# Kernel tuning notes

Measured on AMD Instinct MI355X. Metric: run time of the kernel, lower is better.

Reference implementation:

```python
import jax, jax.numpy as jnp
import numpy as np

# Irreps config: input/output = 32x0e + 16x1o (dim 80), H=4 heads -> head = 8x0e + 4x1o (dim 20)
M0, M1 = 32, 16      # input muls for 0e / 1o
m0, m1 = 8, 4        # per-head muls
H = 4
HEAD_DIM = m0 + 3 * m1   # 20
WNUM = H * (M0 * m0 + M1 * m0 + M0 * m1 + M1 * m1)  # 2304 per-edge TP weights
NB, HID = 16, 64
SQRT3 = np.float32(np.sqrt(3.0))
EPS = 1e-8


def radial_mlp(x, W1, b1, W2, b2):
    return jax.nn.silu(x @ W1 + b1) @ W2 + b2


def tp_edge(ss, vv, sh0, sh1, w):
    """FullyConnectedTensorProduct (32x0e+16x1o) x (1x0e+1x1o) -> H*(8x0e+4x1o) with per-edge weights w [E, WNUM].
    Paths: 0e*0e->0e, 1o*1o->0e (CG dot/sqrt3), 0e*1o->1o, 1o*0e->1o; path norm 1/sqrt(fan_in)."""
    E = ss.shape[0]
    per = M0 * m0 + M1 * m0 + M0 * m1 + M1 * m1  # 576
    w = w.reshape(E, H, per)
    o = 0
    Wss = w[..., o:o + M0 * m0].reshape(E, H, M0, m0); o += M0 * m0
    Wvv = w[..., o:o + M1 * m0].reshape(E, H, M1, m0); o += M1 * m0
    Wsv = w[..., o:o + M0 * m1].reshape(E, H, M0, m1); o += M0 * m1
    Wvs = w[..., o:o + M1 * m1].reshape(E, H, M1, m1)
    fan = np.float32(np.sqrt(M0 + M1))  # fan_in = 48 for both output irreps
    vv_dot = jnp.einsum('eui,ei->eu', vv, sh1) / SQRT3
    out0 = (jnp.einsum('eu,ehuw->ehw', ss * sh0[:, None], Wss)
            + jnp.einsum('eu,ehuw->ehw', vv_dot, Wvv)) / fan          # [E,H,m0]
    out1 = (jnp.einsum('eu,ehuw->ehw', ss, Wsv)[..., None] * sh1[:, None, None, :]
            + jnp.einsum('eui,ehuw->ehwi', vv * sh0[:, None, None], Wvs)) / fan  # [E,H,m1,3]
    return out0, out1


def setup_inputs() -> dict:
    key = jax.random.key(0)
    ks = jax.random.split(key, 24)
    N, E = 2000, 32000
    g = lambda k, s, sc=1.0: jax.random.normal(k, s, jnp.float32) * sc
    inp = {}
    inp['node_features'] = g(ks[0], (N, M0 + 3 * M1))
    inp['edge_index'] = jax.random.randint(ks[1], (2, E), 0, N)
    inp['edge_sh'] = g(ks[2], (E, 4))
    inp['edge_radial_emb'] = jax.random.uniform(ks[3], (E, NB), jnp.float32)
    # query e3nn Linear (per-head blocks)
    inp['Wq0'] = g(ks[4], (H, M0, m0))
    inp['Wq1'] = g(ks[5], (H, M1, m1))
    # radial MLPs for key / value TP weights
    inp['Wk1'] = g(ks[6], (NB, HID), 1 / np.sqrt(NB)); inp['bk1'] = jnp.zeros((HID,), jnp.float32)
    inp['Wk2'] = g(ks[7], (HID, WNUM), 1 / np.sqrt(HID)); inp['bk2'] = jnp.zeros((WNUM,), jnp.float32)
    inp['Wv1'] = g(ks[8], (NB, HID), 1 / np.sqrt(NB)); inp['bv1'] = jnp.zeros((HID,), jnp.float32)
    inp['Wv2'] = g(ks[9], (HID, WNUM), 1 / np.sqrt(HID)); inp['bv2'] = jnp.zeros((WNUM,), jnp.float32)
    # single-head dot-product TP -> 0e (shared weights)
    inp['Wd0'] = g(ks[10], (m0, m0))
    inp['Wd1'] = g(ks[11], (m1, m1))
    # output projection Linear (all heads mixed per irrep)
    inp['Wo0'] = g(ks[12], (H * m0, M0))
    inp['Wo1'] = g(ks[13], (H * m1, M1))
    # FFN: out irreps -> (2*M0)x0e + M1x1o -> out irreps
    inp['Wf1_0'] = g(ks[14], (M0, 2 * M0))
    inp['Wf1_1'] = g(ks[15], (M1, M1))
    inp['Wf2_0'] = g(ks[16], (2 * M0, M0))
    inp['Wf2_1'] = g(ks[17], (M1, M1))
    return inp


def reference(node_features, edge_index, edge_sh, edge_radial_emb,
              Wq0, Wq1, Wk1, bk1, Wk2, bk2, Wv1, bv1, Wv2, bv2,
              Wd0, Wd1, Wo0, Wo1, Wf1_0, Wf1_1, Wf2_0, Wf2_1):
    N = node_features.shape[0]
    s = node_features[:, :M0]                       # [N, M0] scalars
    v = node_features[:, M0:].reshape(N, M1, 3)     # [N, M1, 3] vectors
    src, dst = edge_index[0], edge_index[1]

    # query Linear (e3nn: per-irrep channel mix, norm 1/sqrt(fan_in))
    q0 = jnp.einsum('nu,huw->nhw', s, Wq0) / np.sqrt(M0)
    q1 = jnp.einsum('nui,huw->nhwi', v, Wq1) / np.sqrt(M1)

    sh0, sh1 = edge_sh[:, 0], edge_sh[:, 1:4]
    ss, vv = s[src], v[src]                         # gather per edge

    wk = radial_mlp(edge_radial_emb, Wk1, bk1, Wk2, bk2)
    wv = radial_mlp(edge_radial_emb, Wv1, bv1, Wv2, bv2)
    k0, k1 = tp_edge(ss, vv, sh0, sh1, wk)
    v0, v1 = tp_edge(ss, vv, sh0, sh1, wv)

    # per-head equivariant dot product -> 0e logits
    qd0, qd1 = q0[dst], q1[dst]
    fan_d = np.float32(np.sqrt(m0 * m0 + m1 * m1))
    logits = (jnp.einsum('ehu,uv,ehv->eh', qd0, Wd0, k0)
              + jnp.einsum('ehui,uv,ehvi->eh', qd1, Wd1, k1) / SQRT3) / fan_d
    logits = logits / np.sqrt(HEAD_DIM)             # self.scale
    logits = jnp.clip(logits, -10.0, 10.0)

    # scatter softmax over edges sharing a destination node
    seg_max = jax.ops.segment_max(logits, dst, num_segments=N)
    seg_max = jnp.maximum(seg_max, -10.0)           # handle empty segments
    ex = jnp.exp(logits - seg_max[dst])
    denom = jax.ops.segment_sum(ex, dst, num_segments=N)
    alpha = ex / (denom[dst] + 1e-12)               # [E, H]

    agg0 = jax.ops.segment_sum(alpha[..., None] * v0, dst, num_segments=N)        # [N,H,m0]
    agg1 = jax.ops.segment_sum(alpha[..., None, None] * v1, dst, num_segments=N)  # [N,H,m1,3]

    # output projection Linear over concatenated heads
    o0 = agg0.reshape(N, H * m0) @ Wo0 / np.sqrt(H * m0)
    o1 = jnp.einsum('nui,uw->nwi', agg1.reshape(N, H * m1, 3), Wo1) / np.sqrt(H * m1)

    # residual (input irreps == output irreps -> identity skip)
    x0 = s + o0
    x1 = v + o1

    # FFN with SafeNormActivation
    f0 = x0 @ Wf1_0 / np.sqrt(M0)                               # [N, 2*M0]
    f1 = jnp.einsum('nui,uw->nwi', x1, Wf1_1) / np.sqrt(M1)     # [N, M1, 3]
    a0 = jax.nn.silu(f0)
    norms = jnp.linalg.norm(f1, axis=-1, keepdims=True)
    safe = jnp.maximum(norms, EPS)
    a1 = jnp.where(norms < EPS, 0.0, (f1 / safe) * jax.nn.silu(norms))
    g0 = a0 @ Wf2_0 / np.sqrt(2 * M0)
    g1 = jnp.einsum('nui,uw->nwi', a1, Wf2_1) / np.sqrt(M1)

    out0 = x0 + g0
    out1 = x1 + g1
    return jnp.concatenate([out0, out1.reshape(N, M1 * 3)], axis=-1)
```

## Files before the change

### kernel.cpp

```cpp
#include <hip/hip_runtime.h>

typedef unsigned int uint;
typedef unsigned short ushort;
typedef __attribute__((ext_vector_type(8))) short bf16x8;
typedef __attribute__((ext_vector_type(4))) float f32x4;
typedef __attribute__((ext_vector_type(2))) float f32x2;

#define N_NODES 2000
#define N_EDGES 32000
#define WNUM 2304

constexpr size_t OFF_AGG0 = 0;
constexpr size_t OFF_AGG1 = 64000;
constexpr size_t OFF_DEN  = 160000;
constexpr size_t OFF_CNT  = 168000;
constexpr size_t OFF_FLAG = 170000;
constexpr size_t OFF_W2T  = 170004;
constexpr size_t OFF_QT0  = 317460;
constexpr size_t OFF_QT1  = 381460;
constexpr size_t OFF_EORD = 477460;
constexpr size_t OFF_W1T  = 509460;
constexpr size_t OFF_W1P  = 511508;

__device__ __forceinline__ float b2f(ushort u){ union{uint i; float f;}x; x.i=((uint)u)<<16; return x.f; }
__device__ __forceinline__ float lo16(uint w){ union{uint u; float f;}x; x.u=w<<16; return x.f; }
__device__ __forceinline__ float hi16(uint w){ union{uint u; float f;}x; x.u=w&0xFFFF0000u; return x.f; }
__device__ __forceinline__ ushort f2b(float f){
  union{float f; uint u;}x; x.f=f;
  uint r = (x.u + 0x7FFFu + ((x.u>>16)&1u)) >> 16;
  return (ushort)r;
}
__device__ __forceinline__ float siluf(float x){ return x / (1.f + __expf(-x)); }

template<bool F32>
__device__ __forceinline__ float ldf(const void* p, int i){
  if (F32) return ((const float*)p)[i];
  return b2f(((const ushort*)p)[i]);
}
__device__ __forceinline__ float ldfr(const void* p, int i, bool f32){
  return f32 ? ((const float*)p)[i] : b2f(((const ushort*)p)[i]);
}

template<bool F32>
__device__ void prep_body(
    const void* __restrict__ nf, const int* __restrict__ eidx,
    const void* __restrict__ Wk2, const void* __restrict__ Wv2,
    const void* __restrict__ Wk1, const void* __restrict__ Wv1,
    const void* __restrict__ Wq0, const void* __restrict__ Wq1,
    const void* __restrict__ Wd0, const void* __restrict__ Wd1,
    ushort* __restrict__ W2T, float* __restrict__ W1T, uint* __restrict__ W1P,
    float* __restrict__ qt0, float* __restrict__ qt1,
    int* __restrict__ cnt){
  const int t = threadIdx.x;
  const int bid = blockIdx.x;

  if (bid < 72){
    __shared__ ushort tile[64][66];
    const int mat = bid / 36, jt = bid - mat*36;
    const void* W = mat ? Wv2 : Wk2;
    const int j0 = jt*64;
    const int jo = t & 63, cb = t >> 6;
    #pragma unroll
    for (int k=0; k<16; ++k){
      const int c = cb + k*4;
      tile[c][jo] = F32 ? f2b(((const float*)W)[(size_t)c*WNUM + j0 + jo])
                        : ((const ushort*)W)[(size_t)c*WNUM + j0 + jo];
    }
    __syncthreads();
    const int jl = t >> 2, c0 = (t & 3)*16;
    ushort* dst = W2T + (size_t)mat*147456 + (size_t)(j0+jl)*64 + c0;
    #pragma unroll
    for (int k=0; k<16; ++k) dst[k] = tile[c0+k][jl];
  } else if (bid < 104){
    __shared__ float nfL[64][80];
    __shared__ float wq0L[1024], wq1L[256], wd0L[64], wd1L[16];
    const int nb = bid - 72, n0 = nb*64;
    for (int idx=t; idx<64*80; idx+=256){
      const int nn = n0 + idx/80;
      nfL[idx/80][idx%80] = (nn < N_NODES) ? ldf<F32>(nf, nn*80 + idx%80) : 0.f;
    }
    for (int idx=t; idx<1024; idx+=256) wq0L[idx] = ldf<F32>(Wq0, idx);
    if (t < 256) wq1L[t] = ldf<F32>(Wq1, t);
    if (t < 64)  wd0L[t] = ldf<F32>(Wd0, t);
    if (t < 16)  wd1L[t] = ldf<F32>(Wd1, t);
    __syncthreads();
    const int nl = t >> 2, h = t & 3;
    const int nn = n0 + nl;
    if (nn < N_NODES){
      const float* S = &nfL[nl][0];
      float q0[8];
      #pragma unroll
      for (int w=0; w<8; ++w){
        float a = 0.f;
        #pragma unroll
        for (int u=0; u<32; ++u) a += S[u]*wq0L[h*256 + u*8 + w];
        q0[w] = a * 0.17677669529663687f;
      }
      #pragma unroll
      for (int vv=0; vv<8; ++vv){
        float a = 0.f;
        #pragma unroll
        for (int u=0; u<8; ++u) a += q0[u]*wd0L[u*8+vv];
        qt0[nn*32 + h*8 + vv] = a;
      }
      float q1[12];
      #pragma unroll
      for (int w=0; w<4; ++w)
        #pragma unroll
        for (int i=0; i<3; ++i){
          float a = 0.f;
          #pragma unroll
          for (int u=0; u<16; ++u) a += S[32+u*3+i]*wq1L[h*64 + u*4 + w];
          q1[w*3+i] = a * 0.25f;
        }
      #pragma unroll
      for (int vv=0; vv<4; ++vv)
        #pragma unroll
        for (int i=0; i<3; ++i){
          float a = 0.f;
          #pragma unroll
          for (int u=0; u<4; ++u) a += q1[u*3+i]*wd1L[u*4+vv];
          qt1[nn*48 + h*12 + vv*3 + i] = a;
        }
    }
  } else if (bid == 104){
    for (int idx=t; idx<2048; idx+=256){
      const int mat = idx >> 10, rem = idx & 1023;
      const int c = rem >> 4, b = rem & 15;
      W1T[idx] = ldf<F32>(mat ? Wv1 : Wk1, b*64 + c);
    }
    for (int idx=t; idx<1024; idx+=256){
      const int mat = idx >> 9, rem = idx & 511;
      const int c = rem >> 3, j = rem & 7;
      const void* W = mat ? Wv1 : Wk1;
      ushort u0, u1;
      if (F32){ u0 = f2b(((const float*)W)[(2*j)*64+c]); u1 = f2b(((const float*)W)[(2*j+1)*64+c]); }
      else    { u0 = ((const ushort*)W)[(2*j)*64+c];     u1 = ((const ushort*)W)[(2*j+1)*64+c]; }
      W1P[idx] = (uint)u0 | ((uint)u1 << 16);
    }
  } else {
    const int e = (bid-105)*256 + t;
    if (e < N_EDGES) atomicAdd(cnt + eidx[N_EDGES + e], 1);
  }
}

__global__ __launch_bounds__(256) void prep_kernel(
    const void* nf, const int* eidx,
    const void* Wk2, const void* Wv2,
    const void* Wk1, const void* Wv1,
    const void* Wq0, const void* Wq1,
    const void* Wd0, const void* Wd1,
    ushort* W2T, float* W1T, uint* W1P, float* qt0, float* qt1,
    int* cnt, int* flag){
  __shared__ int s_cnt;
  const int t = threadIdx.x;
  if (t == 0) s_cnt = 0;
  __syncthreads();
  {
    uint u = ((const ushort*)nf)[t*2];
    uint ex = (u >> 7) & 0xFFu;
    if (ex >= 0xA0u) atomicAdd(&s_cnt, 1);
  }
  __syncthreads();
  const bool F32 = (s_cnt >= 20);
  if (blockIdx.x == 0 && t == 0) *flag = F32 ? 1 : 0;
  if (F32) prep_body<true >(nf, eidx, Wk2, Wv2, Wk1, Wv1, Wq0, Wq1, Wd0, Wd1, W2T, W1T, W1P, qt0, qt1, cnt);
  else     prep_body<false>(nf, eidx, Wk2, Wv2, Wk1, Wv1, Wq0, Wq1, Wd0, Wd1, W2T, W1T, W1P, qt0, qt1, cnt);
}

__global__ __launch_bounds__(256) void scan_kernel(int* __restrict__ cnt){
  __shared__ int ls[256];
  const int t = threadIdx.x;
  const int base = t*8;
  int v[8]; int s = 0;
  #pragma unroll
  for (int k=0; k<8; ++k){ int idx = base+k; v[k] = (idx < N_NODES) ? cnt[idx] : 0; s += v[k]; }
  ls[t] = s; __syncthreads();
  for (int off=1; off<256; off<<=1){
    int x = (t >= off) ? ls[t-off] : 0;
    __syncthreads();
    ls[t] += x;
    __syncthreads();
  }
  int ex = ls[t] - s;
  #pragma unroll
  for (int k=0; k<8; ++k){ int idx = base+k; if (idx < N_NODES){ int c = v[k]; cnt[idx] = ex; ex += c; } }
}

__global__ __launch_bounds__(256) void scat_kernel(const int* __restrict__ eidx,
                                                   int* __restrict__ cnt, int* __restrict__ eord){
  int e = blockIdx.x*256 + threadIdx.x;
  if (e < N_EDGES){
    int p = atomicAdd(cnt + eidx[N_EDGES + e], 1);
    eord[p] = e;
  }
}

struct Smem {
  ushort hidA[4096];
  union {
    struct {
      float fssT[32][34];
      float fvvT[16][34];
      float sslT[32][34];
    } f;
    float cont[2688];
  } u;
  float vshT[3][16][34];
  float sh1T[3][34];
  int   dstL[32];
};

template<bool F32>
__device__ void edge_body(
    const void* __restrict__ nf,  const int* __restrict__ eidx,
    const int* __restrict__ eord,
    const void* __restrict__ esh, const void* __restrict__ emb,
    const float* __restrict__ W1T, const uint* __restrict__ W1P,
    const void* __restrict__ bk1, const void* __restrict__ bk2,
    const void* __restrict__ bv1, const void* __restrict__ bv2,
    const ushort* __restrict__ W2T,
    const float* __restrict__ qt0g, const float* __restrict__ qt1g,
    float* __restrict__ agg0, float* __restrict__ agg1, float* __restrict__ denom,
    Smem& sm){
  const int t  = threadIdx.x;
  const int hw = t >> 5;
  const int r  = t & 31;
  const int geb = blockIdx.x*32;

  int geA[4], srcA[4], dstA[4];
  float shv0[4], shv1[4], shv2[4], shv3[4];
  #pragma unroll
  for (int e=0; e<4; ++e) geA[e] = eord[geb + hw*4 + e];
  #pragma unroll
  for (int e=0; e<4; ++e){ srcA[e] = eidx[geA[e]]; dstA[e] = eidx[N_EDGES + geA[e]]; }
  #pragma unroll
  for (int e=0; e<4; ++e){
    if (F32){
      float4 s4 = ((const float4*)esh)[geA[e]];
      shv0[e]=s4.x; shv1[e]=s4.y; shv2[e]=s4.z; shv3[e]=s4.w;
    } else {
      uint2 u2 = ((const uint2*)esh)[geA[e]];
      shv0[e]=lo16(u2.x); shv1[e]=hi16(u2.x); shv2[e]=lo16(u2.y); shv3[e]=hi16(u2.y);
    }
  }
  #pragma unroll
  for (int e=0; e<4; ++e){
    const int le = hw*4+e, src = srcA[e];
    const float sh0 = shv0[e], s1a = shv1[e], s1b = shv2[e], s1c = shv3[e];
    if (r == 0) sm.dstL[le] = dstA[e];
    if (r < 3) sm.sh1T[r][le] = (r==0)? s1a : (r==1)? s1b : s1c;
    float sv = ldf<F32>(nf, src*80 + r);
    sm.u.f.sslT[r][le] = sv;
    sm.u.f.fssT[r][le] = sv * sh0;
    if (r < 16){
      float v0 = ldf<F32>(nf, src*80+32+r*3+0);
      float v1 = ldf<F32>(nf, src*80+32+r*3+1);
      float v2 = ldf<F32>(nf, src*80+32+r*3+2);
      sm.vshT[0][r][le] = v0*sh0; sm.vshT[1][r][le] = v1*sh0; sm.vshT[2][r][le] = v2*sh0;
      sm.u.f.fvvT[r][le] = (v0*s1a + v1*s1b + v2*s1c) * 0.5773502691896258f;
    }
  }

  {
    float bkv[2], bvv[2];
    f32x4 wkF[2][4], wvF[2][4];
    uint4 wkB[2][2], wvB[2][2];
    #pragma unroll
    for (int cc=0; cc<2; ++cc){
      const int c = r + cc*32;
      bkv[cc] = ldf<F32>(bk1, c); bvv[cc] = ldf<F32>(bv1, c);
      if (F32){
        const f32x4* pk = (const f32x4*)(W1T + c*16);
        const f32x4* pv = (const f32x4*)(W1T + 1024 + c*16);
        wkF[cc][0]=pk[0]; wkF[cc][1]=pk[1]; wkF[cc][2]=pk[2]; wkF[cc][3]=pk[3];
        wvF[cc][0]=pv[0]; wvF[cc][1]=pv[1]; wvF[cc][2]=pv[2]; wvF[cc][3]=pv[3];
      } else {
        const uint4* pk = (const uint4*)(W1P + c*8);
        const uint4* pv = (const uint4*)(W1P + 512 + c*8);
        wkB[cc][0]=pk[0]; wkB[cc][1]=pk[1];
        wvB[cc][0]=pv[0]; wvB[cc][1]=pv[1];
      }
    }
    uint4 ra, rb; float4 fa, fb, fc, fd;
    if (F32){
      const float4* p = (const float4*)emb + (size_t)geA[0]*4;
      fa = p[0]; fb = p[1]; fc = p[2]; fd = p[3];
    } else {
      const uint4* p = (const uint4*)emb + (size_t)geA[0]*2;
      ra = p[0]; rb = p[1];
    }
    #pragma unroll
    for (int e=0; e<4; ++e){
      float em[16];
      if (F32){
        em[0]=fa.x; em[1]=fa.y; em[2]=fa.z; em[3]=fa.w;
        em[4]=fb.x; em[5]=fb.y; em[6]=fb.z; em[7]=fb.w;
        em[8]=fc.x; em[9]=fc.y; em[10]=fc.z; em[11]=fc.w;
        em[12]=fd.x; em[13]=fd.y; em[14]=fd.z; em[15]=fd.w;
      } else {
        em[0]=lo16(ra.x); em[1]=hi16(ra.x); em[2]=lo16(ra.y); em[3]=hi16(ra.y);
        em[4]=lo16(ra.z); em[5]=hi16(ra.z); em[6]=lo16(ra.w); em[7]=hi16(ra.w);
        em[8]=lo16(rb.x); em[9]=hi16(rb.x); em[10]=lo16(rb.y); em[11]=hi16(rb.y);
        em[12]=lo16(rb.z); em[13]=hi16(rb.z); em[14]=lo16(rb.w); em[15]=hi16(rb.w);
      }
      if (e < 3){
        if (F32){
          const float4* p = (const float4*)emb + (size_t)geA[e+1]*4;
          fa = p[0]; fb = p[1]; fc = p[2]; fd = p[3];
        } else {
          const uint4* p = (const uint4*)emb + (size_t)geA[e+1]*2;
          ra = p[0]; rb = p[1];
        }
      }
      const int le = hw*4+e;
      #pragma unroll
      for (int cc=0; cc<2; ++cc){
        const int c = r + cc*32;
        float ak = bkv[cc], av = bvv[cc];
        if (F32){
          #pragma unroll
          for (int g=0; g<4; ++g)
            #pragma unroll
            for (int j=0; j<4; ++j){
              ak += em[g*4+j]*wkF[cc][g][j];
              av += em[g*4+j]*wvF[cc][g][j];
            }
        } else {
          #pragma unroll
          for (int g=0; g<2; ++g){
            const uint4 a = wkB[cc][g], b = wvB[cc][g];
            ak += em[g*8+0]*lo16(a.x) + em[g*8+1]*hi16(a.x)
                + em[g*8+2]*lo16(a.y) + em[g*8+3]*hi16(a.y)
                + em[g*8+4]*lo16(a.z) + em[g*8+5]*hi16(a.z)
                + em[g*8+6]*lo16(a.w) + em[g*8+7]*hi16(a.w);
            av += em[g*8+0]*lo16(b.x) + em[g*8+1]*hi16(b.x)
                + em[g*8+2]*lo16(b.y) + em[g*8+3]*hi16(b.y)
                + em[g*8+4]*lo16(b.z) + em[g*8+5]*hi16(b.z)
                + em[g*8+6]*lo16(b.w) + em[g*8+7]*hi16(b.w);
          }
        }
        const int idx = (le>>4)*1024 + (c>>5)*512 + ((((c>>3)&3)*16 + (le&15))<<3) + (c&7);
        sm.hidA[idx]        = f2b(siluf(ak));
        sm.hidA[2048 + idx] = f2b(siluf(av));
      }
    }
  }
  __syncthreads();

  const int h = t >> 6;
  const int lane = t & 63, q = lane >> 4, n = lane & 15;
  const float invfan = 0.14433756729740643f;
  float exv[2][4];

  const ushort* wbase = W2T + h*36864 + n*64 + q*8;
  const int bi0 = h*576 + n;
  const float* fb_ss = &sm.u.f.fssT[n>>3][q*4];
  const float* fb_sl = &sm.u.f.sslT[n>>2][q*4];
  const int nq2 = n>>2;

  #pragma unroll 1
  for (int kv=0; kv<2; ++kv){
    const ushort* wptr = wbase + kv*147456;
    const void* bvec = kv ? bv2 : bk2;
    bf16x8 af[2][2];
    #pragma unroll
    for (int Mt=0; Mt<2; ++Mt)
      #pragma unroll
      for (int kh=0; kh<2; ++kh)
        af[Mt][kh] = *(const bf16x8*)&sm.hidA[kv*2048 + Mt*1024 + kh*512 + lane*8];

    float a0[2][4], aP[2][4], aW[3][2][4];
    #pragma unroll
    for (int Mt=0; Mt<2; ++Mt)
      #pragma unroll
      for (int z=0; z<4; ++z){
        a0[Mt][z]=0.f; aP[Mt][z]=0.f;
        aW[0][Mt][z]=0.f; aW[1][Mt][z]=0.f; aW[2][Mt][z]=0.f;
      }

    bf16x8 pb0 = *(const bf16x8*)(wptr);
    bf16x8 pb1 = *(const bf16x8*)(wptr + 32);
    float pbb = ldf<F32>(bvec, bi0);

    #pragma unroll 4
    for (int tl=0; tl<24; ++tl){
      bf16x8 b0 = pb0, b1 = pb1; const float bb = pbb;
      pb0 = *(const bf16x8*)(wptr + (tl+1)*1024);
      pb1 = *(const bf16x8*)(wptr + (tl+1)*1024 + 32);
      pbb = ldf<F32>(bvec, bi0 + (tl+1)*16);
      const float* fp = fb_ss + tl*68;
      #pragma unroll
      for (int Mt=0; Mt<2; ++Mt){
        f32x4 c = {bb,bb,bb,bb};
        c = __builtin_amdgcn_mfma_f32_16x16x32_bf16(af[Mt][0], b0, c, 0,0,0);
        c = __builtin_amdgcn_mfma_f32_16x16x32_bf16(af[Mt][1], b1, c, 0,0,0);
        f32x2 fA = *(const f32x2*)(fp + Mt*16);
        f32x2 fB = *(const f32x2*)(fp + Mt*16 + 2);
        a0[Mt][0] += c[0]*fA[0]; a0[Mt][1] += c[1]*fA[1];
        a0[Mt][2] += c[2]*fB[0]; a0[Mt][3] += c[3]*fB[1];
      }
    }
    #pragma unroll 4
    for (int tl=24; tl<32; ++tl){
      bf16x8 b0 = pb0, b1 = pb1; const float bb = pbb;
      pb0 = *(const bf16x8*)(wptr + (tl+1)*1024);
      pb1 = *(const bf16x8*)(wptr + (tl+1)*1024 + 32);
      pbb = ldf<F32>(bvec, bi0 + (tl+1)*16);
      const float* fp = fb_sl + (tl-24)*136;
      #pragma unroll
      for (int Mt=0; Mt<2; ++Mt){
        f32x4 c = {bb,bb,bb,bb};
        c = __builtin_amdgcn_mfma_f32_16x16x32_bf16(af[Mt][0], b0, c, 0,0,0);
        c = __builtin_amdgcn_mfma_f32_16x16x32_bf16(af[Mt][1], b1, c, 0,0,0);
        f32x2 fA = *(const f32x2*)(fp + Mt*16);
        f32x2 fB = *(const f32x2*)(fp + Mt*16 + 2);
        aP[Mt][0] += c[0]*fA[0]; aP[Mt][1] += c[1]*fA[1];
        aP[Mt][2] += c[2]*fB[0]; aP[Mt][3] += c[3]*fB[1];
      }
    }
    #pragma unroll
    for (int tl=32; tl<36; ++tl){
      bf16x8 b0 = pb0, b1 = pb1; const float bb = pbb;
      if (tl < 35){
        pb0 = *(const bf16x8*)(wptr + (tl+1)*1024);
        pb1 = *(const bf16x8*)(wptr + (tl+1)*1024 + 32);
        pbb = ldf<F32>(bvec, bi0 + (tl+1)*16);
      }
      const int u = (tl-32)*4 + nq2;
      #pragma unroll
      for (int Mt=0; Mt<2; ++Mt){
        f32x4 c = {bb,bb,bb,bb};
        c = __builtin_amdgcn_mfma_f32_16x16x32_bf16(af[Mt][0], b0, c, 0,0,0);
        c = __builtin_amdgcn_mfma_f32_16x16x32_bf16(af[Mt][1], b1, c, 0,0,0);
        #pragma unroll
        for (int i=0; i<3; ++i){
          f32x2 fA = *(const f32x2*)&sm.vshT[i][u][Mt*16+q*4];
          f32x2 fB = *(const f32x2*)&sm.vshT[i][u][Mt*16+q*4+2];
          aW[i][Mt][0] += c[0]*fA[0]; aW[i][Mt][1] += c[1]*fA[1];
          aW[i][Mt][2] += c[2]*fB[0]; aW[i][Mt][3] += c[3]*fB[1];
        }
      }
    }

    #pragma unroll
    for (int Mt=0; Mt<2; ++Mt)
      #pragma unroll
      for (int z=0; z<4; ++z){
        a0[Mt][z] += __shfl_xor(a0[Mt][z], 8, 64);
        aP[Mt][z] += __shfl_xor(aP[Mt][z], 4, 64);
        aP[Mt][z] += __shfl_xor(aP[Mt][z], 8, 64);
        #pragma unroll
        for (int i=0; i<3; ++i){
          aW[i][Mt][z] += __shfl_xor(aW[i][Mt][z], 4, 64);
          aW[i][Mt][z] += __shfl_xor(aW[i][Mt][z], 8, 64);
        }
      }

    if (kv == 0){
      float lgp[2][4];
      #pragma unroll
      for (int Mt=0; Mt<2; ++Mt)
        #pragma unroll
        for (int z=0; z<4; ++z){
          const int el = Mt*16 + q*4 + z;
          const int d = sm.dstL[el];
          float acc = 0.f;
          if (n < 8) acc = qt0g[d*32 + h*8 + n] * a0[Mt][z];
          if (n < 4){
            float s = 0.f;
            #pragma unroll
            for (int i=0; i<3; ++i){
              float k1 = aP[Mt][z]*sm.sh1T[i][el] + aW[i][Mt][z];
              s += qt1g[d*48 + h*12 + n*3 + i] * k1;
            }
            acc += s * 0.5773502691896258f;
          }
          lgp[Mt][z] = acc;
        }
      #pragma unroll
      for (int Mt=0; Mt<2; ++Mt)
        #pragma unroll
        for (int z=0; z<4; ++z){
          lgp[Mt][z] += __shfl_xor(lgp[Mt][z], 1, 64);
          lgp[Mt][z] += __shfl_xor(lgp[Mt][z], 2, 64);
          lgp[Mt][z] += __shfl_xor(lgp[Mt][z], 4, 64);
          lgp[Mt][z] += __shfl_xor(lgp[Mt][z], 8, 64);
          float lg = lgp[Mt][z] * invfan * 0.025f;
          lg = fminf(10.f, fmaxf(-10.f, lg));
          exv[Mt][z] = __expf(lg - 10.0f);
        }
    } else {
      __syncthreads();
      #pragma unroll
      for (int Mt=0; Mt<2; ++Mt)
        #pragma unroll
        for (int z=0; z<4; ++z){
          const int el = Mt*16 + q*4 + z;
          const float ex = exv[Mt][z];
          float* cp = &sm.u.cont[el*84 + h*21];
          if (n == 0) cp[0] = ex;
          if (n < 8)  cp[1+n] = ex * a0[Mt][z] * invfan;
          if (n < 4){
            #pragma unroll
            for (int i=0; i<3; ++i){
              float v1 = (aP[Mt][z]*sm.sh1T[i][el] + aW[i][Mt][z]) * invfan;
              cp[9+n*3+i] = ex * v1;
            }
          }
        }
    }
  }
  __syncthreads();

  if (t < 168){
    const int half = (t >= 84) ? 1 : 0;
    const int tt = t - half*84;
    const int h2 = tt / 21, comp = tt - h2*21;
    const int e0 = half*16, e1 = e0 + 16;
    float acc = 0.f;
    #pragma unroll 4
    for (int e2=e0; e2<e1; ++e2){
      acc += sm.u.cont[e2*84 + h2*21 + comp];
      const int d2 = sm.dstL[e2];
      if (e2 == e1-1 || sm.dstL[e2+1] != d2){
        if (comp == 0)      atomicAdd(denom + d2*4  + h2, acc);
        else if (comp < 9)  atomicAdd(agg0  + d2*32 + h2*8  + (comp-1), acc);
        else                atomicAdd(agg1  + d2*48 + h2*12 + (comp-9), acc);
        acc = 0.f;
      }
    }
  }
}

__global__ __launch_bounds__(256) void edge_kernel(
    const void* nf, const int* eidx, const int* eord, const void* esh, const void* emb,
    const float* W1T, const uint* W1P,
    const void* bk1, const void* bk2,
    const void* bv1, const void* bv2,
    const ushort* W2T, const float* qt0g, const float* qt1g,
    float* agg0, float* agg1, float* denom, const int* flag){
  __shared__ Smem sm;
  if (*flag)
    edge_body<true >(nf,eidx,eord,esh,emb,W1T,W1P,bk1,bk2,bv1,bv2,W2T,qt0g,qt1g,agg0,agg1,denom,sm);
  else
    edge_body<false>(nf,eidx,eord,esh,emb,W1T,W1P,bk1,bk2,bv1,bv2,W2T,qt0g,qt1g,agg0,agg1,denom,sm);
}

__global__ __launch_bounds__(256) void node_out_kernel(
    const void* __restrict__ nf, const float* __restrict__ agg0r, const float* __restrict__ agg1r,
    const float* __restrict__ denom,
    const void* __restrict__ Wo0, const void* __restrict__ Wo1,
    const void* __restrict__ Wf10, const void* __restrict__ Wf11,
    const void* __restrict__ Wf20, const void* __restrict__ Wf21,
    void* __restrict__ out, const int* __restrict__ flag){
  __shared__ float ag0[4][32], ag1[4][48], adiv[4][4];
  __shared__ float x0s[4][32], x1s[4][48], a0s[4][64], f1s[4][48], coefs[4][16];
  const bool F32 = (*flag) != 0;
  const int s = threadIdx.x >> 6, t = threadIdx.x & 63;
  const int n = blockIdx.x*4 + s;
  if (t < 4) adiv[s][t] = 1.f / (denom[n*4+t] + 1e-12f);
  __syncthreads();
  if (t < 32) ag0[s][t] = agg0r[n*32+t] * adiv[s][t>>3];
  if (t < 48) ag1[s][t] = agg1r[n*48+t] * adiv[s][t/12];
  __syncthreads();
  if (t < 32){
    float o = 0.f;
    #pragma unroll
    for (int k=0; k<32; ++k) o += ag0[s][k]*ldfr(Wo0, k*32+t, F32);
    x0s[s][t] = ldfr(nf, n*80+t, F32) + o*0.17677669529663687f;
  }
  if (t < 48){
    int w = t/3, i = t - w*3;
    float o = 0.f;
    #pragma unroll
    for (int u=0; u<16; ++u) o += ag1[s][u*3+i]*ldfr(Wo1, u*16+w, F32);
    x1s[s][t] = ldfr(nf, n*80+32+t, F32) + o*0.25f;
  }
  __syncthreads();
  {
    float f0 = 0.f;
    #pragma unroll
    for (int u=0; u<32; ++u) f0 += x0s[s][u]*ldfr(Wf10, u*64+t, F32);
    a0s[s][t] = siluf(f0*0.17677669529663687f);
  }
  if (t < 48){
    int w = t/3, i = t - w*3;
    float f1 = 0.f;
    #pragma unroll
    for (int u=0; u<16; ++u) f1 += x1s[s][u*3+i]*ldfr(Wf11, u*16+w, F32);
    f1s[s][t] = f1*0.25f;
  }
  __syncthreads();
  if (t < 16){
    float a = f1s[s][t*3], b = f1s[s][t*3+1], c = f1s[s][t*3+2];
    float nrm = sqrtf(a*a+b*b+c*c);
    float safe = fmaxf(nrm, 1e-8f);
    coefs[s][t] = (nrm < 1e-8f) ? 0.f : siluf(nrm)/safe;
  }
  __syncthreads();
  if (t < 32){
    float g = 0.f;
    #pragma unroll
    for (int u=0; u<64; ++u) g += a0s[s][u]*ldfr(Wf20, u*32+t, F32);
    float val = x0s[s][t] + g*0.125f;
    if (F32) ((float*)out)[n*80+t] = val; else ((ushort*)out)[n*80+t] = f2b(val);
  }
  if (t < 48){
    int w = t/3, i = t - w*3;
    float g = 0.f;
    #pragma unroll
    for (int u=0; u<16; ++u) g += coefs[s][u]*f1s[s][u*3+i]*ldfr(Wf21, u*16+w, F32);
    float val = x1s[s][t] + g*0.25f;
    if (F32) ((float*)out)[n*80+32+t] = val; else ((ushort*)out)[n*80+32+t] = f2b(val);
  }
}

extern "C" void kernel_launch(void* const* d_in, const int* in_sizes, int n_in,
                              void* d_out, int out_size, void* d_ws, size_t ws_size,
                              hipStream_t stream){
  const void* nf   = d_in[0];
  const int*  eidx = (const int*)d_in[1];
  const void* esh  = d_in[2];
  const void* emb  = d_in[3];
  const void* Wq0  = d_in[4];
  const void* Wq1  = d_in[5];
  const void* Wk1  = d_in[6];
  const void* bk1  = d_in[7];
  const void* Wk2  = d_in[8];
  const void* bk2  = d_in[9];
  const void* Wv1  = d_in[10];
  const void* bv1  = d_in[11];
  const void* Wv2  = d_in[12];
  const void* bv2  = d_in[13];
  const void* Wd0  = d_in[14];
  const void* Wd1  = d_in[15];
  const void* Wo0  = d_in[16];
  const void* Wo1  = d_in[17];
  const void* Wf10 = d_in[18];
  const void* Wf11 = d_in[19];
  const void* Wf20 = d_in[20];
  const void* Wf21 = d_in[21];
  float* ws = (float*)d_ws;

  float* agg0  = ws + OFF_AGG0;
  float* agg1  = ws + OFF_AGG1;
  float* denom = ws + OFF_DEN;
  int*   cnt   = (int*)(ws + OFF_CNT);
  int*   flag  = (int*)(ws + OFF_FLAG);
  ushort* W2T  = (ushort*)(ws + OFF_W2T);
  float* qt0   = ws + OFF_QT0;
  float* qt1   = ws + OFF_QT1;
  int*   eord  = (int*)(ws + OFF_EORD);
  float* W1T   = ws + OFF_W1T;
  uint*  W1P   = (uint*)(ws + OFF_W1P);

  hipMemsetAsync(agg0, 0, 170000*sizeof(float), stream);
  prep_kernel<<<230, 256, 0, stream>>>(nf, eidx, Wk2, Wv2, Wk1, Wv1, Wq0, Wq1, Wd0, Wd1,
                                       W2T, W1T, W1P, qt0, qt1, cnt, flag);
  scan_kernel<<<1, 256, 0, stream>>>(cnt);
  scat_kernel<<<125, 256, 0, stream>>>(eidx, cnt, eord);
  edge_kernel<<<N_EDGES/32, 256, 0, stream>>>(nf, eidx, eord, esh, emb,
                                              W1T, W1P, bk1, bk2, bv1, bv2,
                                              W2T, qt0, qt1,
                                              agg0, agg1, denom, flag);
  node_out_kernel<<<N_NODES/4, 256, 0, stream>>>(nf, agg0, agg1, denom,
                                                 Wo0, Wo1, Wf10, Wf11, Wf20, Wf21, d_out, flag);
}
```

Measured before the change: 226.0 us.

## Split key/value TP passes across separate wavefronts with 512-thread edge blocks

The edge kernel grows from 256 to 512 threads per block. Key and value weight passes now run concurrently on separate wave groups instead of a serial kv loop, and the logits from the key waves reach the value waves through a new shared exL array. The prologue and hidden-layer work is redistributed over the larger block, the weight prefetch is double-buffered, and the final segment reduction uses four edge ranges instead of two. This doubles parallelism per block and shortens the serial chain, but raises register and LDS pressure per block, which may lower occupancy.

```diff
diff --git a/kernel.cpp b/kernel.cpp
--- a/kernel.cpp
+++ b/kernel.cpp
@@ -208,8 +208,23 @@
   } u;
   float vshT[3][16][34];
   float sh1T[3][34];
+  float exL[32][4];
   int   dstL[32];
 };
+
+__device__ __forceinline__ f32x4 mma_pair(const bf16x8& a0f, const bf16x8& a1f,
+                                          bf16x8 b0, bf16x8 b1, float bb){
+  f32x4 c = {bb,bb,bb,bb};
+  c = __builtin_amdgcn_mfma_f32_16x16x32_bf16(a0f, b0, c, 0,0,0);
+  c = __builtin_amdgcn_mfma_f32_16x16x32_bf16(a1f, b1, c, 0,0,0);
+  return c;
+}
+__device__ __forceinline__ void acc_feat(const f32x4 c, const float* fp, float* acc){
+  f32x2 fA = *(const f32x2*)(fp);
+  f32x2 fB = *(const f32x2*)(fp + 2);
+  acc[0] += c[0]*fA[0]; acc[1] += c[1]*fA[1];
+  acc[2] += c[2]*fB[0]; acc[3] += c[3]*fB[1];
+}
 
 template<bool F32>
 __device__ void edge_body(
@@ -224,70 +239,72 @@
     float* __restrict__ agg0, float* __restrict__ agg1, float* __restrict__ denom,
     Smem& sm){
   const int t  = threadIdx.x;
-  const int hw = t >> 5;
-  const int r  = t & 31;
   const int geb = blockIdx.x*32;
 
-  int geA[4], srcA[4], dstA[4];
-  float shv0[4], shv1[4], shv2[4], shv3[4];
-  #pragma unroll
-  for (int e=0; e<4; ++e) geA[e] = eord[geb + hw*4 + e];
-  #pragma unroll
-  for (int e=0; e<4; ++e){ srcA[e] = eidx[geA[e]]; dstA[e] = eidx[N_EDGES + geA[e]]; }
-  #pragma unroll
-  for (int e=0; e<4; ++e){
+  {
+    const int g = t >> 5, r = t & 31;
+    int geA[2], srcA[2], dstA[2];
+    float shv0[2], shv1[2], shv2[2], shv3[2];
+    #pragma unroll
+    for (int e=0; e<2; ++e) geA[e] = eord[geb + g*2 + e];
+    #pragma unroll
+    for (int e=0; e<2; ++e){ srcA[e] = eidx[geA[e]]; dstA[e] = eidx[N_EDGES + geA[e]]; }
+    #pragma unroll
+    for (int e=0; e<2; ++e){
+      if (F32){
+        float4 s4 = ((const float4*)esh)[geA[e]];
+        shv0[e]=s4.x; shv1[e]=s4.y; shv2[e]=s4.z; shv3[e]=s4.w;
+      } else {
+        uint2 u2 = ((const uint2*)esh)[geA[e]];
+        shv0[e]=lo16(u2.x); shv1[e]=hi16(u2.x); shv2[e]=lo16(u2.y); shv3[e]=hi16(u2.y);
+      }
+    }
+    #pragma unroll
+    for (int e=0; e<2; ++e){
+      const int le = g*2+e, src = srcA[e];
+      const float sh0 = shv0[e], s1a = shv1[e], s1b = shv2[e], s1c = shv3[e];
+      if (r == 0) sm.dstL[le] = dstA[e];
+      if (r < 3) sm.sh1T[r][le] = (r==0)? s1a : (r==1)? s1b : s1c;
+      float sv = ldf<F32>(nf, src*80 + r);
+      sm.u.f.sslT[r][le] = sv;
+      sm.u.f.fssT[r][le] = sv * sh0;
+      if (r < 16){
+        float v0 = ldf<F32>(nf, src*80+32+r*3+0);
+        float v1 = ldf<F32>(nf, src*80+32+r*3+1);
+        float v2 = ldf<F32>(nf, src*80+32+r*3+2);
+        sm.vshT[0][r][le] = v0*sh0; sm.vshT[1][r][le] = v1*sh0; sm.vshT[2][r][le] = v2*sh0;
+        sm.u.f.fvvT[r][le] = (v0*s1a + v1*s1b + v2*s1c) * 0.5773502691896258f;
+      }
+    }
+  }
+
+  {
+    const int c  = t & 63;
+    const int g4 = t >> 6;
+    int geB[4];
+    #pragma unroll
+    for (int e=0; e<4; ++e) geB[e] = eord[geb + g4*4 + e];
+
+    float bkv = ldf<F32>(bk1, c), bvv = ldf<F32>(bv1, c);
+    f32x4 wkF[4], wvF[4];
+    uint4 wkB[2], wvB[2];
     if (F32){
-      float4 s4 = ((const float4*)esh)[geA[e]];
-      shv0[e]=s4.x; shv1[e]=s4.y; shv2[e]=s4.z; shv3[e]=s4.w;
+      const f32x4* pk = (const f32x4*)(W1T + c*16);
+      const f32x4* pv = (const f32x4*)(W1T + 1024 + c*16);
+      wkF[0]=pk[0]; wkF[1]=pk[1]; wkF[2]=pk[2]; wkF[3]=pk[3];
+      wvF[0]=pv[0]; wvF[1]=pv[1]; wvF[2]=pv[2]; wvF[3]=pv[3];
     } else {
-      uint2 u2 = ((const uint2*)esh)[geA[e]];
-      shv0[e]=lo16(u2.x); shv1[e]=hi16(u2.x); shv2[e]=lo16(u2.y); shv3[e]=hi16(u2.y);
-    }
-  }
-  #pragma unroll
-  for (int e=0; e<4; ++e){
-    const int le = hw*4+e, src = srcA[e];
-    const float sh0 = shv0[e], s1a = shv1[e], s1b = shv2[e], s1c = shv3[e];
-    if (r == 0) sm.dstL[le] = dstA[e];
-    if (r < 3) sm.sh1T[r][le] = (r==0)? s1a : (r==1)? s1b : s1c;
-    float sv = ldf<F32>(nf, src*80 + r);
-    sm.u.f.sslT[r][le] = sv;
-    sm.u.f.fssT[r][le] = sv * sh0;
-    if (r < 16){
-      float v0 = ldf<F32>(nf, src*80+32+r*3+0);
-      float v1 = ldf<F32>(nf, src*80+32+r*3+1);
-      float v2 = ldf<F32>(nf, src*80+32+r*3+2);
-      sm.vshT[0][r][le] = v0*sh0; sm.vshT[1][r][le] = v1*sh0; sm.vshT[2][r][le] = v2*sh0;
-      sm.u.f.fvvT[r][le] = (v0*s1a + v1*s1b + v2*s1c) * 0.5773502691896258f;
-    }
-  }
-
-  {
-    float bkv[2], bvv[2];
-    f32x4 wkF[2][4], wvF[2][4];
-    uint4 wkB[2][2], wvB[2][2];
-    #pragma unroll
-    for (int cc=0; cc<2; ++cc){
-      const int c = r + cc*32;
-      bkv[cc] = ldf<F32>(bk1, c); bvv[cc] = ldf<F32>(bv1, c);
-      if (F32){
-        const f32x4* pk = (const f32x4*)(W1T + c*16);
-        const f32x4* pv = (const f32x4*)(W1T + 1024 + c*16);
-        wkF[cc][0]=pk[0]; wkF[cc][1]=pk[1]; wkF[cc][2]=pk[2]; wkF[cc][3]=pk[3];
-        wvF[cc][0]=pv[0]; wvF[cc][1]=pv[1]; wvF[cc][2]=pv[2]; wvF[cc][3]=pv[3];
-      } else {
-        const uint4* pk = (const uint4*)(W1P + c*8);
-        const uint4* pv = (const uint4*)(W1P + 512 + c*8);
-        wkB[cc][0]=pk[0]; wkB[cc][1]=pk[1];
-        wvB[cc][0]=pv[0]; wvB[cc][1]=pv[1];
-      }
+      const uint4* pk = (const uint4*)(W1P + c*8);
+      const uint4* pv = (const uint4*)(W1P + 512 + c*8);
+      wkB[0]=pk[0]; wkB[1]=pk[1];
+      wvB[0]=pv[0]; wvB[1]=pv[1];
     }
     uint4 ra, rb; float4 fa, fb, fc, fd;
     if (F32){
-      const float4* p = (const float4*)emb + (size_t)geA[0]*4;
+      const float4* p = (const float4*)emb + (size_t)geB[0]*4;
       fa = p[0]; fb = p[1]; fc = p[2]; fd = p[3];
     } else {
-      const uint4* p = (const uint4*)emb + (size_t)geA[0]*2;
+      const uint4* p = (const uint4*)emb + (size_t)geB[0]*2;
       ra = p[0]; rb = p[1];
     }
     #pragma unroll
@@ -306,218 +323,206 @@
       }
       if (e < 3){
         if (F32){
-          const float4* p = (const float4*)emb + (size_t)geA[e+1]*4;
+          const float4* p = (const float4*)emb + (size_t)geB[e+1]*4;
           fa = p[0]; fb = p[1]; fc = p[2]; fd = p[3];
         } else {
-          const uint4* p = (const uint4*)emb + (size_t)geA[e+1]*2;
+          const uint4* p = (const uint4*)emb + (size_t)geB[e+1]*2;
           ra = p[0]; rb = p[1];
         }
       }
-      const int le = hw*4+e;
-      #pragma unroll
-      for (int cc=0; cc<2; ++cc){
-        const int c = r + cc*32;
-        float ak = bkv[cc], av = bvv[cc];
-        if (F32){
+      const int le = g4*4+e;
+      float ak = bkv, av = bvv;
+      if (F32){
+        #pragma unroll
+        for (int g=0; g<4; ++g)
           #pragma unroll
-          for (int g=0; g<4; ++g)
-            #pragma unroll
-            for (int j=0; j<4; ++j){
-              ak += em[g*4+j]*wkF[cc][g][j];
-              av += em[g*4+j]*wvF[cc][g][j];
-            }
-        } else {
-          #pragma unroll
-          for (int g=0; g<2; ++g){
-            const uint4 a = wkB[cc][g], b = wvB[cc][g];
-            ak += em[g*8+0]*lo16(a.x) + em[g*8+1]*hi16(a.x)
-                + em[g*8+2]*lo16(a.y) + em[g*8+3]*hi16(a.y)
-                + em[g*8+4]*lo16(a.z) + em[g*8+5]*hi16(a.z)
-                + em[g*8+6]*lo16(a.w) + em[g*8+7]*hi16(a.w);
-            av += em[g*8+0]*lo16(b.x) + em[g*8+1]*hi16(b.x)
-                + em[g*8+2]*lo16(b.y) + em[g*8+3]*hi16(b.y)
-                + em[g*8+4]*lo16(b.z) + em[g*8+5]*hi16(b.z)
-                + em[g*8+6]*lo16(b.w) + em[g*8+7]*hi16(b.w);
+          for (int j=0; j<4; ++j){
+            ak += em[g*4+j]*wkF[g][j];
+            av += em[g*4+j]*wvF[g][j];
           }
+      } else {
+        #pragma unroll
+        for (int g=0; g<2; ++g){
+          const uint4 a = wkB[g], b = wvB[g];
+          ak += em[g*8+0]*lo16(a.x) + em[g*8+1]*hi16(a.x)
+              + em[g*8+2]*lo16(a.y) + em[g*8+3]*hi16(a.y)
+              + em[g*8+4]*lo16(a.z) + em[g*8+5]*hi16(a.z)
+              + em[g*8+6]*lo16(a.w) + em[g*8+7]*hi16(a.w);
+          av += em[g*8+0]*lo16(b.x) + em[g*8+1]*hi16(b.x)
+              + em[g*8+2]*lo16(b.y) + em[g*8+3]*hi16(b.y)
+              + em[g*8+4]*lo16(b.z) + em[g*8+5]*hi16(b.z)
+              + em[g*8+6]*lo16(b.w) + em[g*8+7]*hi16(b.w);
         }
-        const int idx = (le>>4)*1024 + (c>>5)*512 + ((((c>>3)&3)*16 + (le&15))<<3) + (c&7);
-        sm.hidA[idx]        = f2b(siluf(ak));
-        sm.hidA[2048 + idx] = f2b(siluf(av));
-      }
-    }
-  }
-  __syncthreads();
-
-  const int h = t >> 6;
+      }
+      const int idx = (le>>4)*1024 + (c>>5)*512 + ((((c>>3)&3)*16 + (le&15))<<3) + (c&7);
+      sm.hidA[idx]        = f2b(siluf(ak));
+      sm.hidA[2048 + idx] = f2b(siluf(av));
+    }
+  }
+  __syncthreads();
+
+  const int w  = t >> 6;
+  const int kv = w >> 2;
+  const int h  = w & 3;
   const int lane = t & 63, q = lane >> 4, n = lane & 15;
   const float invfan = 0.14433756729740643f;
-  float exv[2][4];
-
-  const ushort* wbase = W2T + h*36864 + n*64 + q*8;
+
+  const ushort* wptr = W2T + (size_t)kv*147456 + h*36864 + n*64 + q*8;
+  const void* bvec = kv ? bv2 : bk2;
   const int bi0 = h*576 + n;
   const float* fb_ss = &sm.u.f.fssT[n>>3][q*4];
   const float* fb_sl = &sm.u.f.sslT[n>>2][q*4];
   const int nq2 = n>>2;
 
-  #pragma unroll 1
-  for (int kv=0; kv<2; ++kv){
-    const ushort* wptr = wbase + kv*147456;
-    const void* bvec = kv ? bv2 : bk2;
-    bf16x8 af[2][2];
+  bf16x8 af[2][2];
+  #pragma unroll
+  for (int Mt=0; Mt<2; ++Mt)
+    #pragma unroll
+    for (int kh=0; kh<2; ++kh)
+      af[Mt][kh] = *(const bf16x8*)&sm.hidA[kv*2048 + Mt*1024 + kh*512 + lane*8];
+
+  float a0[2][4], aP[2][4], aW[3][2][4];
+  #pragma unroll
+  for (int Mt=0; Mt<2; ++Mt)
+    #pragma unroll
+    for (int z=0; z<4; ++z){
+      a0[Mt][z]=0.f; aP[Mt][z]=0.f;
+      aW[0][Mt][z]=0.f; aW[1][Mt][z]=0.f; aW[2][Mt][z]=0.f;
+    }
+
+#define PREF(P0,P1,PB,TL) \
+  P0 = *(const bf16x8*)(wptr + (TL)*1024); \
+  P1 = *(const bf16x8*)(wptr + (TL)*1024 + 32); \
+  PB = ldf<F32>(bvec, bi0 + (TL)*16);
+
+  bf16x8 pA0, pA1, pB0, pB1; float pAb, pBb;
+  PREF(pA0, pA1, pAb, 0);
+  PREF(pB0, pB1, pBb, 1);
+
+  #pragma unroll 2
+  for (int tl=0; tl<24; tl+=2){
+    { bf16x8 b0=pA0, b1=pA1; float bb=pAb;
+      PREF(pA0, pA1, pAb, tl+2);
+      const float* fp = fb_ss + tl*68;
+      #pragma unroll
+      for (int Mt=0; Mt<2; ++Mt) acc_feat(mma_pair(af[Mt][0], af[Mt][1], b0, b1, bb), fp + Mt*16, a0[Mt]); }
+    { bf16x8 b0=pB0, b1=pB1; float bb=pBb;
+      PREF(pB0, pB1, pBb, tl+3);
+      const float* fp = fb_ss + (tl+1)*68;
+      #pragma unroll
+      for (int Mt=0; Mt<2; ++Mt) acc_feat(mma_pair(af[Mt][0], af[Mt][1], b0, b1, bb), fp + Mt*16, a0[Mt]); }
+  }
+  #pragma unroll 2
+  for (int tl=24; tl<32; tl+=2){
+    { bf16x8 b0=pA0, b1=pA1; float bb=pAb;
+      PREF(pA0, pA1, pAb, tl+2);
+      const float* fp = fb_sl + (tl-24)*136;
+      #pragma unroll
+      for (int Mt=0; Mt<2; ++Mt) acc_feat(mma_pair(af[Mt][0], af[Mt][1], b0, b1, bb), fp + Mt*16, aP[Mt]); }
+    { bf16x8 b0=pB0, b1=pB1; float bb=pBb;
+      PREF(pB0, pB1, pBb, tl+3);
+      const float* fp = fb_sl + (tl-23)*136;
+      #pragma unroll
+      for (int Mt=0; Mt<2; ++Mt) acc_feat(mma_pair(af[Mt][0], af[Mt][1], b0, b1, bb), fp + Mt*16, aP[Mt]); }
+  }
+#define BODY_AW(B0,B1,BB,TL) { \
+    const int u = ((TL)-32)*4 + nq2; \
+    _Pragma("unroll") \
+    for (int Mt=0; Mt<2; ++Mt){ \
+      f32x4 c = mma_pair(af[Mt][0], af[Mt][1], B0, B1, BB); \
+      _Pragma("unroll") \
+      for (int i=0; i<3; ++i) acc_feat(c, &sm.vshT[i][u][Mt*16+q*4], aW[i][Mt]); \
+    } }
+  { bf16x8 b0=pA0, b1=pA1; float bb=pAb; PREF(pA0, pA1, pAb, 34); BODY_AW(b0,b1,bb,32); }
+  { bf16x8 b0=pB0, b1=pB1; float bb=pBb; PREF(pB0, pB1, pBb, 35); BODY_AW(b0,b1,bb,33); }
+  { bf16x8 b0=pA0, b1=pA1; float bb=pAb; BODY_AW(b0,b1,bb,34); }
+  { bf16x8 b0=pB0, b1=pB1; float bb=pBb; BODY_AW(b0,b1,bb,35); }
+#undef BODY_AW
+#undef PREF
+
+  #pragma unroll
+  for (int Mt=0; Mt<2; ++Mt)
+    #pragma unroll
+    for (int z=0; z<4; ++z){
+      a0[Mt][z] += __shfl_xor(a0[Mt][z], 8, 64);
+      aP[Mt][z] += __shfl_xor(aP[Mt][z], 4, 64);
+      aP[Mt][z] += __shfl_xor(aP[Mt][z], 8, 64);
+      #pragma unroll
+      for (int i=0; i<3; ++i){
+        aW[i][Mt][z] += __shfl_xor(aW[i][Mt][z], 4, 64);
+        aW[i][Mt][z] += __shfl_xor(aW[i][Mt][z], 8, 64);
+      }
+    }
+
+  if (kv == 0){
+    float lgp[2][4];
     #pragma unroll
     for (int Mt=0; Mt<2; ++Mt)
       #pragma unroll
-      for (int kh=0; kh<2; ++kh)
-        af[Mt][kh] = *(const bf16x8*)&sm.hidA[kv*2048 + Mt*1024 + kh*512 + lane*8];
-
-    float a0[2][4], aP[2][4], aW[3][2][4];
+      for (int z=0; z<4; ++z){
+        const int el = Mt*16 + q*4 + z;
+        const int d = sm.dstL[el];
+        float acc = 0.f;
+        if (n < 8) acc = qt0g[d*32 + h*8 + n] * a0[Mt][z];
+        if (n < 4){
+          float s = 0.f;
+          #pragma unroll
+          for (int i=0; i<3; ++i){
+            float k1 = aP[Mt][z]*sm.sh1T[i][el] + aW[i][Mt][z];
+            s += qt1g[d*48 + h*12 + n*3 + i] * k1;
+          }
+          acc += s * 0.5773502691896258f;
+        }
+        lgp[Mt][z] = acc;
+      }
     #pragma unroll
     for (int Mt=0; Mt<2; ++Mt)
       #pragma unroll
       for (int z=0; z<4; ++z){
-        a0[Mt][z]=0.f; aP[Mt][z]=0.f;
-        aW[0][Mt][z]=0.f; aW[1][Mt][z]=0.f; aW[2][Mt][z]=0.f;
-      }
-
-    bf16x8 pb0 = *(const bf16x8*)(wptr);
-    bf16x8 pb1 = *(const bf16x8*)(wptr + 32);
-    float pbb = ldf<F32>(bvec, bi0);
-
-    #pragma unroll 4
-    for (int tl=0; tl<24; ++tl){
-      bf16x8 b0 = pb0, b1 = pb1; const float bb = pbb;
-      pb0 = *(const bf16x8*)(wptr + (tl+1)*1024);
-      pb1 = *(const bf16x8*)(wptr + (tl+1)*1024 + 32);
-      pbb = ldf<F32>(bvec, bi0 + (tl+1)*16);
-      const float* fp = fb_ss + tl*68;
-      #pragma unroll
-      for (int Mt=0; Mt<2; ++Mt){
-        f32x4 c = {bb,bb,bb,bb};
-        c = __builtin_amdgcn_mfma_f32_16x16x32_bf16(af[Mt][0], b0, c, 0,0,0);
-        c = __builtin_amdgcn_mfma_f32_16x16x32_bf16(af[Mt][1], b1, c, 0,0,0);
-        f32x2 fA = *(const f32x2*)(fp + Mt*16);
-        f32x2 fB = *(const f32x2*)(fp + Mt*16 + 2);
-        a0[Mt][0] += c[0]*fA[0]; a0[Mt][1] += c[1]*fA[1];
-        a0[Mt][2] += c[2]*fB[0]; a0[Mt][3] += c[3]*fB[1];
-      }
-    }
-    #pragma unroll 4
-    for (int tl=24; tl<32; ++tl){
-      bf16x8 b0 = pb0, b1 = pb1; const float bb = pbb;
-      pb0 = *(const bf16x8*)(wptr + (tl+1)*1024);
-      pb1 = *(const bf16x8*)(wptr + (tl+1)*1024 + 32);
-      pbb = ldf<F32>(bvec, bi0 + (tl+1)*16);
-      const float* fp = fb_sl + (tl-24)*136;
-      #pragma unroll
-      for (int Mt=0; Mt<2; ++Mt){
-        f32x4 c = {bb,bb,bb,bb};
-        c = __builtin_amdgcn_mfma_f32_16x16x32_bf16(af[Mt][0], b0, c, 0,0,0);
-        c = __builtin_amdgcn_mfma_f32_16x16x32_bf16(af[Mt][1], b1, c, 0,0,0);
-        f32x2 fA = *(const f32x2*)(fp + Mt*16);
-        f32x2 fB = *(const f32x2*)(fp + Mt*16 + 2);
-        aP[Mt][0] += c[0]*fA[0]; aP[Mt][1] += c[1]*fA[1];
-        aP[Mt][2] += c[2]*fB[0]; aP[Mt][3] += c[3]*fB[1];
-      }
-    }
-    #pragma unroll
-    for (int tl=32; tl<36; ++tl){
-      bf16x8 b0 = pb0, b1 = pb1; const float bb = pbb;
-      if (tl < 35){
-        pb0 = *(const bf16x8*)(wptr + (tl+1)*1024);
-        pb1 = *(const bf16x8*)(wptr + (tl+1)*1024 + 32);
-        pbb = ldf<F32>(bvec, bi0 + (tl+1)*16);
-      }
-      const int u = (tl-32)*4 + nq2;
-      #pragma unroll
-      for (int Mt=0; Mt<2; ++Mt){
-        f32x4 c = {bb,bb,bb,bb};
-        c = __builtin_amdgcn_mfma_f32_16x16x32_bf16(af[Mt][0], b0, c, 0,0,0);
-        c = __builtin_amdgcn_mfma_f32_16x16x32_bf16(af[Mt][1], b1, c, 0,0,0);
-        #pragma unroll
-        for (int i=0; i<3; ++i){
-          f32x2 fA = *(const f32x2*)&sm.vshT[i][u][Mt*16+q*4];
-          f32x2 fB = *(const f32x2*)&sm.vshT[i][u][Mt*16+q*4+2];
-          aW[i][Mt][0] += c[0]*fA[0]; aW[i][Mt][1] += c[1]*fA[1];
-          aW[i][Mt][2] += c[2]*fB[0]; aW[i][Mt][3] += c[3]*fB[1];
-        }
-      }
-    }
-
-    #pragma unroll
-    for (int Mt=0; Mt<2; ++Mt)
-      #pragma unroll
-      for (int z=0; z<4; ++z){
-        a0[Mt][z] += __shfl_xor(a0[Mt][z], 8, 64);
-        aP[Mt][z] += __shfl_xor(aP[Mt][z], 4, 64);
-        aP[Mt][z] += __shfl_xor(aP[Mt][z], 8, 64);
-        #pragma unroll
-        for (int i=0; i<3; ++i){
-          aW[i][Mt][z] += __shfl_xor(aW[i][Mt][z], 4, 64);
-          aW[i][Mt][z] += __shfl_xor(aW[i][Mt][z], 8, 64);
-        }
-      }
-
-    if (kv == 0){
-      float lgp[2][4];
+        lgp[Mt][z] += __shfl_xor(lgp[Mt][z], 1, 64);
+        lgp[Mt][z] += __shfl_xor(lgp[Mt][z], 2, 64);
+        lgp[Mt][z] += __shfl_xor(lgp[Mt][z], 4, 64);
+        lgp[Mt][z] += __shfl_xor(lgp[Mt][z], 8, 64);
+      }
+    if (n == 0){
       #pragma unroll
       for (int Mt=0; Mt<2; ++Mt)
         #pragma unroll
         for (int z=0; z<4; ++z){
-          const int el = Mt*16 + q*4 + z;
-          const int d = sm.dstL[el];
-          float acc = 0.f;
-          if (n < 8) acc = qt0g[d*32 + h*8 + n] * a0[Mt][z];
-          if (n < 4){
-            float s = 0.f;
-            #pragma unroll
-            for (int i=0; i<3; ++i){
-              float k1 = aP[Mt][z]*sm.sh1T[i][el] + aW[i][Mt][z];
-              s += qt1g[d*48 + h*12 + n*3 + i] * k1;
-            }
-            acc += s * 0.5773502691896258f;
-          }
-          lgp[Mt][z] = acc;
-        }
-      #pragma unroll
-      for (int Mt=0; Mt<2; ++Mt)
-        #pragma unroll
-        for (int z=0; z<4; ++z){
-          lgp[Mt][z] += __shfl_xor(lgp[Mt][z], 1, 64);
-          lgp[Mt][z] += __shfl_xor(lgp[Mt][z], 2, 64);
-          lgp[Mt][z] += __shfl_xor(lgp[Mt][z], 4, 64);
-          lgp[Mt][z] += __shfl_xor(lgp[Mt][z], 8, 64);
           float lg = lgp[Mt][z] * invfan * 0.025f;
           lg = fminf(10.f, fmaxf(-10.f, lg));
-          exv[Mt][z] = __expf(lg - 10.0f);
+          sm.exL[Mt*16 + q*4 + z][h] = __expf(lg - 10.0f);
         }
-    } else {
-      __syncthreads();
-      #pragma unroll
-      for (int Mt=0; Mt<2; ++Mt)
-        #pragma unroll
-        for (int z=0; z<4; ++z){
-          const int el = Mt*16 + q*4 + z;
-          const float ex = exv[Mt][z];
-          float* cp = &sm.u.cont[el*84 + h*21];
-          if (n == 0) cp[0] = ex;
-          if (n < 8)  cp[1+n] = ex * a0[Mt][z] * invfan;
-          if (n < 4){
-            #pragma unroll
-            for (int i=0; i<3; ++i){
-              float v1 = (aP[Mt][z]*sm.sh1T[i][el] + aW[i][Mt][z]) * invfan;
-              cp[9+n*3+i] = ex * v1;
-            }
+    }
+  }
+  __syncthreads();
+
+  if (kv == 1){
+    #pragma unroll
+    for (int Mt=0; Mt<2; ++Mt)
+      #pragma unroll
+      for (int z=0; z<4; ++z){
+        const int el = Mt*16 + q*4 + z;
+        const float ex = sm.exL[el][h];
+        float* cp = &sm.u.cont[el*84 + h*21];
+        if (n == 0) cp[0] = ex;
+        if (n < 8)  cp[1+n] = ex * a0[Mt][z] * invfan;
+        if (n < 4){
+          #pragma unroll
+          for (int i=0; i<3; ++i){
+            float v1 = (aP[Mt][z]*sm.sh1T[i][el] + aW[i][Mt][z]) * invfan;
+            cp[9+n*3+i] = ex * v1;
           }
         }
-    }
-  }
-  __syncthreads();
-
-  if (t < 168){
-    const int half = (t >= 84) ? 1 : 0;
-    const int tt = t - half*84;
+      }
+  }
+  __syncthreads();
+
+  if (t < 336){
+    const int quarter = t / 84;
+    const int tt = t - quarter*84;
     const int h2 = tt / 21, comp = tt - h2*21;
-    const int e0 = half*16, e1 = e0 + 16;
+    const int e0 = quarter*8, e1 = e0 + 8;
     float acc = 0.f;
     #pragma unroll 4
     for (int e2=e0; e2<e1; ++e2){
@@ -533,7 +538,7 @@
   }
 }
 
-__global__ __launch_bounds__(256) void edge_kernel(
+__global__ __launch_bounds__(512) void edge_kernel(
     const void* nf, const int* eidx, const int* eord, const void* esh, const void* emb,
     const float* W1T, const uint* W1P,
     const void* bk1, const void* bk2,
@@ -660,7 +665,7 @@
                                        W2T, W1T, W1P, qt0, qt1, cnt, flag);
   scan_kernel<<<1, 256, 0, stream>>>(cnt);
   scat_kernel<<<125, 256, 0, stream>>>(eidx, cnt, eord);
-  edge_kernel<<<N_EDGES/32, 256, 0, stream>>>(nf, eidx, eord, esh, emb,
+  edge_kernel<<<N_EDGES/32, 512, 0, stream>>>(nf, eidx, eord, esh, emb,
                                               W1T, W1P, bk1, bk2, bv1, bv2,
                                               W2T, qt0, qt1,
                                               agg0, agg1, denom, flag);
```

New measurement: 235.5 us. 1.04x slower.
